# Optimization experiments

Measured on AMD Instinct MI355X. Metric: run time of the kernel, lower is better.

The kernel has to match this reference:

```python
import jax, jax.numpy as jnp
import numpy as np

N, F_IN, HID, NCLS, E = 100000, 256, 256, 32, 3200000
NHEADS, HDIM, MFEAT = 4, 64, 266  # MFEAT = int(HDIM * ln(HDIM)), performer default
ALPHA, KSTEPS, EPS = 0.1, 10, 1e-4


def setup_inputs() -> dict:
    key = jax.random.key(0)
    ks = jax.random.split(key, 16)
    p = lambda k, sh: (jax.random.normal(k, sh, dtype=jnp.float32) * 0.02)
    return {
        "x": jax.random.normal(ks[0], (N, F_IN), dtype=jnp.float32),
        "edge_index": jax.random.randint(ks[1], (2, E), 0, N, dtype=jnp.int64),
        "lin1_w": p(ks[2], (HID, F_IN)), "lin1_b": p(ks[3], (HID,)),
        "lin2_w": p(ks[4], (NCLS, 2 * HID)), "lin2_b": p(ks[5], (NCLS,)),
        "q_w": p(ks[6], (HID, F_IN)), "q_b": p(ks[7], (HID,)),
        "k_w": p(ks[8], (HID, F_IN)), "k_b": p(ks[9], (HID,)),
        "v_w": p(ks[10], (HID, F_IN)), "v_b": p(ks[11], (HID,)),
        "proj": jax.random.normal(ks[12], (MFEAT, HDIM), dtype=jnp.float32),
    }


def _softmax_kernel(data, proj, is_query):
    # performer_pytorch softmax random-feature map
    d = data.shape[-1]
    m = proj.shape[0]
    dn = d ** -0.25
    ratio = m ** -0.5
    data_dash = jnp.einsum('bhnd,md->bhnm', data * dn, proj)
    diag = 0.5 * (dn ** 2) * jnp.sum(data * data, axis=-1, keepdims=True)  # [b,h,n,1]
    if is_query:
        mx = jax.lax.stop_gradient(jnp.max(data_dash, axis=-1, keepdims=True))
    else:
        mx = jax.lax.stop_gradient(jnp.max(data_dash, axis=(-2, -1), keepdims=True))
    return ratio * (jnp.exp(data_dash - diag - mx) + EPS)


def _fast_attention(q, k, v, proj):
    # non-causal performer linear attention; q,k,v: [b,h,n,d]
    qp = _softmax_kernel(q, proj, True)   # [b,h,n,m]
    kp = _softmax_kernel(k, proj, False)  # [b,h,n,m]
    k_sum = jnp.sum(kp, axis=-2)                                   # [b,h,m]
    d_inv = 1.0 / jnp.einsum('bhnm,bhm->bhn', qp, k_sum)           # [b,h,n]
    context = jnp.einsum('bhnm,bhnd->bhmd', kp, v)                 # [b,h,m,d]
    return jnp.einsum('bhmd,bhnm,bhn->bhnd', context, qp, d_inv)   # [b,h,n,d]


def _appnp(x, edge_index, n):
    # gcn_norm with self-loops, then K iterations of x <- (1-a) A_hat x + a h
    src = jnp.concatenate([edge_index[0], jnp.arange(n, dtype=edge_index.dtype)])
    dst = jnp.concatenate([edge_index[1], jnp.arange(n, dtype=edge_index.dtype)])
    deg = jax.ops.segment_sum(jnp.ones_like(dst, dtype=x.dtype), dst, num_segments=n)
    dis = jnp.where(deg > 0, jax.lax.rsqrt(deg), 0.0)
    w = (dis[src] * dis[dst])[:, None]  # [E+N, 1]
    h = x
    for _ in range(KSTEPS):
        msg = jax.ops.segment_sum(x[src] * w, dst, num_segments=n)
        x = (1.0 - ALPHA) * msg + ALPHA * h
    return x


def reference(x, edge_index, lin1_w, lin1_b, lin2_w, lin2_b,
              q_w, q_b, k_w, k_b, v_w, v_b, proj):
    n = x.shape[0]
    # dropout layers are identity in eval mode
    xu = x[None]  # [1, N, F]
    q = (xu @ q_w.T + q_b).reshape(1, n, NHEADS, HDIM).transpose(0, 2, 1, 3)
    k = (xu @ k_w.T + k_b).reshape(1, n, NHEADS, HDIM).transpose(0, 2, 1, 3)
    v = (xu @ v_w.T + v_b).reshape(1, n, NHEADS, HDIM).transpose(0, 2, 1, 3)
    attn = _fast_attention(q, k, v, proj)                      # [1,h,n,d]
    trans = attn.transpose(0, 2, 1, 3).reshape(n, HID)         # [N, HID]
    gnn1 = x @ lin1_w.T + lin1_b                               # [N, HID]
    cat = jax.nn.elu(jnp.concatenate([gnn1, trans], axis=1))   # [N, 2*HID]
    gnn2 = jax.nn.elu(cat @ lin2_w.T + lin2_b)                 # [N, NCLS]
    final = _appnp(gnn2, edge_index, n)
    return jax.nn.log_softmax(final, axis=1), final
```

## Files before the change

kernel.cpp:

```cpp
#include <hip/hip_runtime.h>
#include <hip/hip_fp16.h>

#define NH 4
#define HD 64
#define MF 266
#define MP 288
#define NB 192
#define NBQ 128
#define DN 0.35355339059327373f
#define RATIO 0.06131393394849658f
#define EPSRF 1e-4f
#define REPS (RATIO*EPSRF)

typedef unsigned short u16;
typedef unsigned int u32;
typedef __attribute__((ext_vector_type(8))) short bf16x8;
typedef __attribute__((ext_vector_type(4))) float f32x4;
#define MFMA16(a,b,c) __builtin_amdgcn_mfma_f32_16x16x32_bf16(a,b,c,0,0,0)

__device__ __forceinline__ float bf2f(u16 u){ return __uint_as_float(((u32)u)<<16); }
__device__ __forceinline__ u16 f2bf(float f){ u32 u = __float_as_uint(f); u += 0x7FFFu + ((u>>16)&1u); return (u16)(u>>16); }
__device__ __forceinline__ u32 pack2bf(float a, float b){ return ((u32)f2bf(b)<<16) | f2bf(a); }
__device__ __forceinline__ float eluf(float x){ return x>0.f ? x : (expf(x)-1.f); }

__global__ void k_cvtw(const float* __restrict__ qw, const float* __restrict__ kw,
                       const float* __restrict__ vw, const float* __restrict__ lw,
                       const float* __restrict__ l2w, const float* __restrict__ proj,
                       u16* __restrict__ Wb, u16* __restrict__ projp, u16* __restrict__ l2wb){
  int i = blockIdx.x*256 + threadIdx.x;
  if (i < 262144){
    int sec = i>>16, r = i&65535;
    const float* s = sec==0?qw : sec==1?kw : sec==2?vw : lw;
    Wb[i] = f2bf(s[r]);
  }
  if (i < MP*64){
    int r = i>>6, c = i&63;
    projp[i] = f2bf(r < MF ? proj[r*64 + c] : 0.f);
  }
  if (i < 32*512) l2wb[i] = f2bf(l2w[i]);
}

__global__ __launch_bounds__(512,4) void k_proj(
    const float* __restrict__ x, const u16* __restrict__ Wb,
    const float* __restrict__ qb, const float* __restrict__ kb,
    const float* __restrict__ vb, const float* __restrict__ lb,
    u16* __restrict__ Q, u16* __restrict__ K, u16* __restrict__ V,
    u16* __restrict__ G1, int n)
{
  __shared__ u32 Xs[128*128];
  const int tid = threadIdx.x;
  const int w = tid>>6, l = tid&63;
  const int wr = w>>2, wc = w&3;
  const int lm = l&15, lk = l>>4;
  const int row0 = blockIdx.x*128;
  #pragma unroll 4
  for (int q=0;q<16;++q){
    int idx = q*512 + tid;
    int r = idx>>6, c4 = idx&63;
    int rr = row0 + r; if (rr > n-1) rr = n-1;
    float4 v = *(const float4*)(x + (size_t)rr*256 + c4*4);
    int word = (c4*2) ^ ((r&7)<<2);
    *(uint2*)&Xs[r*128 + word] = make_uint2(pack2bf(v.x,v.y), pack2bf(v.z,v.w));
  }
  __syncthreads();
  #pragma unroll 1
  for (int ct=0; ct<8; ++ct){
    const int c0 = ct*128 + wc*32;
    f32x4 acc[4][2] = {};
    #pragma unroll 2
    for (int kt=0; kt<8; ++kt){
      bf16x8 Af[4], Bf[2];
      #pragma unroll
      for (int jj=0;jj<2;jj++)
        Bf[jj] = *(const bf16x8*)(Wb + (size_t)(c0 + jj*16 + lm)*256 + kt*32 + lk*8);
      #pragma unroll
      for (int i=0;i<4;i++){
        const int rl = wr*64 + i*16 + lm;
        Af[i] = *(const bf16x8*)&Xs[rl*128 + ((kt*16 + lk*4) ^ ((rl&7)<<2))];
      }
      #pragma unroll
      for (int i=0;i<4;i++)
        #pragma unroll
        for (int jj=0;jj<2;jj++)
          acc[i][jj] = MFMA16(Af[i], Bf[jj], acc[i][jj]);
    }
    const int sel = c0>>8;
    const float* bp = sel==0?qb : sel==1?kb : sel==2?vb : lb;
    u16* d3 = sel==0?Q : sel==1?K : sel==2?V : G1;
    u32* dst32 = (u32*)d3;
    const bool even = (lm&1)==0;
    #pragma unroll
    for (int jj=0;jj<2;jj++){
      const int cc = (c0&255) + jj*16 + lm;
      const float bias = bp[cc];
      const int ccA = cc & ~1;
      const int hh = ccA>>6, dd = ccA&63;
      #pragma unroll
      for (int i=0;i<4;i++){
        const int rb = row0 + wr*64 + i*16 + lk*4;
        u32 m01 = pack2bf(acc[i][jj][0]+bias, acc[i][jj][1]+bias);
        u32 m23 = pack2bf(acc[i][jj][2]+bias, acc[i][jj][3]+bias);
        u32 oa = __shfl_xor(m01,1);
        u32 ob = __shfl_xor(m23,1);
        u32 wA = even ? ((m01 & 0xffffu) | ((oa & 0xffffu)<<16))
                      : ((ob  & 0xffffu) | ((m23 & 0xffffu)<<16));
        u32 wB = even ? ((m01 >> 16) | (oa & 0xffff0000u))
                      : ((ob  >> 16) | (m23 & 0xffff0000u));
        const int rA = rb + (even ? 0 : 2);
        const int rB = rA + 1;
        if (sel==3){
          if (rA < n) dst32[(size_t)rA*128 + (ccA>>1)] = wA;
          if (rB < n) dst32[(size_t)rB*128 + (ccA>>1)] = wB;
        } else {
          if (rA < n) dst32[(((size_t)hh*n + rA)<<5) + (dd>>1)] = wA;
          if (rB < n) dst32[(((size_t)hh*n + rB)<<5) + (dd>>1)] = wB;
        }
      }
    }
  }
}

__global__ void k_vcs(const u16* __restrict__ Vb, float* __restrict__ vcs, int n){
  const int h = blockIdx.y, tid = threadIdx.x;
  const int d = tid&63, seg = tid>>6;
  float s = 0.f;
  for (int node = blockIdx.x*4 + seg; node < n; node += 256)
    s += bf2f(Vb[(((size_t)h*n + node)<<6) + d]);
  __shared__ float sm[4][64];
  sm[seg][d] = s; __syncthreads();
  if (tid < 64){
    float t2 = sm[0][tid]+sm[1][tid]+sm[2][tid]+sm[3][tid];
    atomicAdd(vcs + h*64 + tid, t2);
  }
}

__global__ __launch_bounds__(256) void k_ctx(
    const u16* __restrict__ Kb, const u16* __restrict__ Vb,
    const u16* __restrict__ projp,
    float* __restrict__ ctxp, float* __restrict__ ksump,
    u32* __restrict__ kmaxg, int n)
{
  __shared__ u32 kpT[288*32];
  __shared__ u16 Vt[64][72];
  __shared__ float redk[4][288];
  const int tid = threadIdx.x;
  const int w = tid>>6, l = tid&63;
  const int bb = blockIdx.x;
  const int h = blockIdx.y;
  const int lm = l&15, lk = l>>4;
  f32x4 cacc[18] = {};
  float ksa[18] = {};
  float mreg = -3.0e38f;
  const int ntile = (n+63)>>6;
  #pragma unroll 1
  for (int t=bb; t<ntile; t+=NB){
    const int n0 = t*64;
    __syncthreads();
    #pragma unroll
    for (int q=0;q<2;q++){
      int e8 = tid + q*256;
      int nn = e8>>3, d0 = (e8&7)*8;
      uint4 rv = make_uint4(0,0,0,0);
      if (n0+nn < n) rv = *(const uint4*)(Vb + (((size_t)h*n + n0+nn)<<6) + d0);
      const u16* pv = (const u16*)&rv;
      #pragma unroll
      for (int s=0;s<8;s++) Vt[d0+s][nn] = pv[s];
    }
    int rr = n0 + w*16 + lm; if (rr > n-1) rr = n-1;
    const u16* Kbase = Kb + (((size_t)h*n + rr)<<6);
    bf16x8 af0 = *(const bf16x8*)(Kbase + lk*8);
    bf16x8 af1 = *(const bf16x8*)(Kbase + 32 + lk*8);
    float dg = 0.f;
    #pragma unroll
    for (int i2=0;i2<8;i2++){
      float a = bf2f(((const u16*)&af0)[i2]);
      float b = bf2f(((const u16*)&af1)[i2]);
      dg += a*a + b*b;
    }
    dg += __shfl_xor(dg,16); dg += __shfl_xor(dg,32);
    dg *= 0.0625f;
    float dgr[4];
    #pragma unroll
    for (int j=0;j<4;j++) dgr[j] = __shfl(dg, lk*4+j, 16);
    #pragma unroll
    for (int mt=0; mt<18; ++mt){
      bf16x8 b0 = *(const bf16x8*)(projp + (size_t)(mt*16+lm)*64 + lk*8);
      bf16x8 b1 = *(const bf16x8*)(projp + (size_t)(mt*16+lm)*64 + 32 + lk*8);
      f32x4 D = {0,0,0,0};
      D = MFMA16(af0, b0, D);
      D = MFMA16(af1, b1, D);
      const int m = mt*16 + lm;
      const bool vm = m < MF;
      float colsum = 0.f;
      u32 pk0 = 0, pk1 = 0;
      #pragma unroll
      for (int j=0;j<4;j++){
        float ddash = DN * D[j];
        float kp = 0.f;
        if (vm && (n0 + w*16 + lk*4 + j) < n){
          kp = RATIO * __expf(ddash - dgr[j]);
          mreg = fmaxf(mreg, ddash);
          colsum += kp;
        }
        if (j<2) pk0 |= ((u32)f2bf(kp)) << (16*j);
        else     pk1 |= ((u32)f2bf(kp)) << (16*(j-2));
      }
      const int wn0 = w*8 + lk*2;
      *(uint2*)&kpT[m*32 + (wn0 ^ ((m&7)<<2))] = make_uint2(pk0, pk1);
      colsum += __shfl_xor(colsum,16); colsum += __shfl_xor(colsum,32);
      ksa[mt] += colsum;
    }
    __syncthreads();
    #pragma unroll
    for (int mt=0; mt<18; ++mt){
      const int m = mt*16 + lm;
      #pragma unroll
      for (int ks=0;ks<2;++ks){
        bf16x8 a = *(const bf16x8*)&kpT[m*32 + ((ks*16 + lk*4) ^ ((m&7)<<2))];
        bf16x8 bv = *(const bf16x8*)&Vt[w*16+lm][ks*32 + lk*8];
        cacc[mt] = MFMA16(a, bv, cacc[mt]);
      }
    }
  }
  float* cp = ctxp + ((size_t)(h*NB + bb))*MP*64;
  #pragma unroll
  for (int mt=0;mt<18;++mt){
    #pragma unroll
    for (int j=0;j<4;j++){
      int m = mt*16 + lk*4 + j;
      cp[(size_t)m*64 + w*16 + lm] = cacc[mt][j];
    }
  }
  if (l < 16){
    #pragma unroll
    for (int mt=0;mt<18;++mt) redk[w][mt*16+lm] = ksa[mt];
  }
  __shared__ float redm[4];
  float mr = mreg;
  #pragma unroll
  for (int s=1;s<64;s<<=1) mr = fmaxf(mr, __shfl_xor(mr, s));
  if (l==0) redm[w] = mr;
  __syncthreads();
  for (int m2=tid; m2<MP; m2+=256){
    float s = redk[0][m2]+redk[1][m2]+redk[2][m2]+redk[3][m2];
    ksump[((size_t)(h*NB+bb))*MP + m2] = s;
  }
  if (tid==0){
    float bm = fmaxf(fmaxf(redm[0],redm[1]), fmaxf(redm[2],redm[3]));
    u32 b = __float_as_uint(bm);
    u32 enc = (b & 0x80000000u) ? ~b : (b | 0x80000000u);
    atomicMax(kmaxg + h, enc);
  }
}

__global__ void k_reduce(const float* __restrict__ ctxp, const float* __restrict__ ksump,
                         const u32* __restrict__ kmaxg, const float* __restrict__ vcs,
                         u16* __restrict__ ctxT, float* __restrict__ ksum, int n)
{
  const int T1 = NH*MP*64;
  int idx = blockIdx.x*256 + threadIdx.x;
  if (idx < T1){
    int h = idx/(MP*64), r = idx - h*MP*64, m = r>>6, d = r&63;
    u32 ee = kmaxg[h]; u32 b = (ee & 0x80000000u) ? (ee ^ 0x80000000u) : ~ee;
    float sc = __expf(-__uint_as_float(b));
    float s = 0.f;
    for (int bb=0; bb<NB; ++bb) s += ctxp[(((size_t)(h*NB+bb))*MP + m)*64 + d];
    float val = (m < MF) ? (sc*s + REPS*vcs[h*64 + d]) : 0.f;
    ctxT[((size_t)h*64 + d)*MP + m] = f2bf(val);
  } else if (idx < T1 + NH*MP){
    int k2 = idx - T1, h = k2/MP, m = k2 - h*MP;
    u32 ee = kmaxg[h]; u32 b = (ee & 0x80000000u) ? (ee ^ 0x80000000u) : ~ee;
    float sc = __expf(-__uint_as_float(b));
    float s = 0.f;
    for (int bb=0; bb<NB; ++bb) s += ksump[((size_t)(h*NB+bb))*MP + m];
    ksum[h*MP + m] = (m < MF) ? (sc*s + REPS*(float)n) : 0.f;
  }
}

__global__ __launch_bounds__(256) void k_qattn(
    const u16* __restrict__ Qb, const u16* __restrict__ projp,
    const u16* __restrict__ ctxT, const float* __restrict__ ksum,
    u16* __restrict__ trans, int n)
{
  __shared__ u32 pj[288*32];
  __shared__ u16 qp_lds[4][16][168];
  const int tid = threadIdx.x;
  const int w = tid>>6, l = tid&63;
  const int h = blockIdx.y;
  const int lm = l&15, lk = l>>4;
  #pragma unroll
  for (int q=0; q<9; ++q){
    int cix = q*256 + tid;
    int row = cix>>3, c4 = (cix&7)*4;
    uint4 v = *(const uint4*)(projp + row*64 + c4*2);
    *(uint4*)&pj[row*32 + (c4 ^ ((row&7)<<2))] = v;
  }
  float ksm[18];
  #pragma unroll
  for (int mt=0;mt<18;++mt) ksm[mt] = ksum[h*MP + mt*16 + lm];
  __syncthreads();
  const int ntile = (n+63)>>6;
  #pragma unroll 1
  for (int t = blockIdx.x; t < ntile; t += NBQ){
    const int nb = t*64 + w*16;
    int rr = nb + lm; if (rr > n-1) rr = n-1;
    const u16* Qbase = Qb + (((size_t)h*n + rr)<<6);
    bf16x8 af0 = *(const bf16x8*)(Qbase + lk*8);
    bf16x8 af1 = *(const bf16x8*)(Qbase + 32 + lk*8);
    float dg = 0.f;
    #pragma unroll
    for (int i2=0;i2<8;i2++){
      float a = bf2f(((const u16*)&af0)[i2]);
      float b = bf2f(((const u16*)&af1)[i2]);
      dg += a*a + b*b;
    }
    dg += __shfl_xor(dg,16); dg += __shfl_xor(dg,32);
    dg *= 0.0625f;
    float dgr[4];
    #pragma unroll
    for (int j=0;j<4;j++) dgr[j] = __shfl(dg, lk*4+j, 16);
    f32x4 D[18];
    #pragma unroll
    for (int mt=0;mt<18;++mt){
      const int m = mt*16 + lm;
      bf16x8 b0 = *(const bf16x8*)&pj[m*32 + ((lk*4) ^ ((m&7)<<2))];
      bf16x8 b1 = *(const bf16x8*)&pj[m*32 + ((16 + lk*4) ^ ((m&7)<<2))];
      f32x4 z = {0,0,0,0};
      z = MFMA16(af0, b0, z);
      z = MFMA16(af1, b1, z);
      D[mt] = z;
    }
    float rmax[4] = {-3.0e38f,-3.0e38f,-3.0e38f,-3.0e38f};
    #pragma unroll
    for (int mt=0;mt<17;++mt){
      const bool vm = (mt<16) || (lm<10);
      #pragma unroll
      for (int j=0;j<4;j++){
        float dd = DN*D[mt][j];
        if (vm) rmax[j] = fmaxf(rmax[j], dd);
      }
    }
    #pragma unroll
    for (int j=0;j<4;j++){
      #pragma unroll
      for (int s=1;s<16;s<<=1) rmax[j] = fmaxf(rmax[j], __shfl_xor(rmax[j], s));
    }
    float den[4] = {0,0,0,0};
    f32x4 o[4] = {{0,0,0,0},{0,0,0,0},{0,0,0,0},{0,0,0,0}};
    #pragma unroll
    for (int mt=0;mt<10;++mt){
      #pragma unroll
      for (int j=0;j<4;j++){
        float qp = RATIO*(__expf(DN*D[mt][j] - dgr[j] - rmax[j]) + EPSRF);
        den[j] += qp * ksm[mt];
        qp_lds[w][lk*4+j][mt*16+lm] = f2bf(qp);
      }
    }
    #pragma unroll
    for (int ks=0;ks<5;++ks){
      bf16x8 av = *(const bf16x8*)&qp_lds[w][lm][ks*32 + lk*8];
      #pragma unroll
      for (int dt=0;dt<4;++dt){
        bf16x8 bv = *(const bf16x8*)(ctxT + (size_t)(h*64 + dt*16 + lm)*MP + ks*32 + lk*8);
        o[dt] = MFMA16(av, bv, o[dt]);
      }
    }
    #pragma unroll
    for (int mt=10;mt<18;++mt){
      #pragma unroll
      for (int j=0;j<4;j++){
        float qp = RATIO*(__expf(DN*D[mt][j] - dgr[j] - rmax[j]) + EPSRF);
        den[j] += qp * ksm[mt];
        qp_lds[w][lk*4+j][(mt-10)*16+lm] = f2bf(qp);
      }
    }
    #pragma unroll
    for (int ks=5;ks<9;++ks){
      bf16x8 av = *(const bf16x8*)&qp_lds[w][lm][(ks-5)*32 + lk*8];
      #pragma unroll
      for (int dt=0;dt<4;++dt){
        bf16x8 bv = *(const bf16x8*)(ctxT + (size_t)(h*64 + dt*16 + lm)*MP + ks*32 + lk*8);
        o[dt] = MFMA16(av, bv, o[dt]);
      }
    }
    #pragma unroll
    for (int j=0;j<4;j++){
      #pragma unroll
      for (int s=1;s<16;s<<=1) den[j] += __shfl_xor(den[j], s);
    }
    #pragma unroll
    for (int j=0;j<4;j++){
      const int node = nb + lk*4 + j;
      if (node < n){
        const float dv = 1.f/den[j];
        #pragma unroll
        for (int dt=0;dt<4;++dt)
          trans[(size_t)node*256 + h*64 + dt*16 + lm] = f2bf(o[dt][j]*dv);
      }
    }
  }
}

__global__ __launch_bounds__(256) void k_gnn2(
    const u16* __restrict__ G1, const u16* __restrict__ trans,
    const u16* __restrict__ l2wb, const float* __restrict__ l2b,
    u16* __restrict__ xb0, int n)
{
  __shared__ u32 cat[64*256];
  const int tid = threadIdx.x;
  const int w = tid>>6, l = tid&63;
  const int lm = l&15, lk = l>>4;
  const int n0 = blockIdx.x*64;
  #pragma unroll
  for (int src=0; src<2; ++src){
    const u16* S = src ? trans : G1;
    #pragma unroll
    for (int q=0;q<8;++q){
      int idx = q*256 + tid;
      int row = idx>>5, v8 = idx&31;
      int rr = n0+row; if (rr > n-1) rr = n-1;
      uint4 raw = *(const uint4*)(S + (size_t)rr*256 + v8*8);
      const u16* p = (const u16*)&raw;
      u32 o2[4];
      #pragma unroll
      for (int t2=0;t2<4;++t2)
        o2[t2] = pack2bf(eluf(bf2f(p[t2*2])), eluf(bf2f(p[t2*2+1])));
      int word = (v8*4 + src*128) ^ ((row&7)<<2);
      *(uint4*)&cat[row*256 + word] = *(uint4*)o2;
    }
  }
  __syncthreads();
  f32x4 acc[2] = {{0,0,0,0},{0,0,0,0}};
  const int rowl = w*16 + lm;
  #pragma unroll 4
  for (int kt=0; kt<16; ++kt){
    bf16x8 a = *(const bf16x8*)&cat[rowl*256 + ((kt*16 + lk*4) ^ ((rowl&7)<<2))];
    #pragma unroll
    for (int jj=0;jj<2;++jj){
      bf16x8 b = *(const bf16x8*)(l2wb + (size_t)(jj*16+lm)*512 + kt*32 + lk*8);
      acc[jj] = MFMA16(a, b, acc[jj]);
    }
  }
  #pragma unroll
  for (int jj=0;jj<2;++jj){
    const int o = jj*16 + lm;
    const float bias = l2b[o];
    #pragma unroll
    for (int jr=0;jr<4;++jr){
      const int node = n0 + w*16 + lk*4 + jr;
      if (node < n)
        xb0[(size_t)node*32 + o] = f2bf(eluf(acc[jj][jr] + bias));
    }
  }
}

__global__ void k_edgemode(const int* __restrict__ ei, int* __restrict__ mode){
  __shared__ int any;
  if (threadIdx.x==0) any = 0;
  __syncthreads();
  if (ei[threadIdx.x*2+1] != 0) any = 1;
  __syncthreads();
  if (threadIdx.x==0) *mode = any;
}
__device__ __forceinline__ int edge_at(const int* ei, int mode, size_t idx){
  if (mode) return ei[idx];
  return (int)((const long long*)ei)[idx];
}

__global__ void k_hist(const int* __restrict__ ei, const int* __restrict__ mode,
                       u32* __restrict__ deg, int e){
  const int md = *mode;
  for (size_t i = (size_t)blockIdx.x*blockDim.x + threadIdx.x; i < (size_t)e; i += (size_t)gridDim.x*blockDim.x)
    atomicAdd(&deg[edge_at(ei, md, (size_t)e + i)], 1u);
}
__global__ void k_dis(const u32* __restrict__ deg, float* __restrict__ dis, int n){
  int i = blockIdx.x*256 + threadIdx.x;
  if (i<n) dis[i] = rsqrtf((float)(deg[i] + 1u));
}
__global__ __launch_bounds__(1024) void k_scan(const u32* __restrict__ deg, u32* __restrict__ rowp, int n){
  __shared__ u32 wsum[16];
  __shared__ u32 carry;
  const int tid = threadIdx.x, lane = tid&63, wv = tid>>6;
  if (tid==0){ carry = 0u; rowp[0] = 0u; }
  __syncthreads();
  for (int base=0; base<n; base+=1024){
    int i = base + tid;
    u32 v = (i<n)? deg[i] : 0u;
    u32 s = v;
    #pragma unroll
    for (int off=1; off<64; off<<=1){
      u32 t = __shfl_up(s, off, 64);
      if (lane >= off) s += t;
    }
    if (lane==63) wsum[wv] = s;
    __syncthreads();
    if (wv==0){
      u32 ws = (lane<16)? wsum[lane] : 0u;
      #pragma unroll
      for (int off=1; off<16; off<<=1){
        u32 t = __shfl_up(ws, off, 64);
        if (lane >= off) ws += t;
      }
      if (lane<16) wsum[lane] = ws;
    }
    __syncthreads();
    u32 pre = carry + (wv ? wsum[wv-1] : 0u);
    if (i<n) rowp[i+1] = pre + s;
    __syncthreads();
    if (tid==0) carry += wsum[15];
    __syncthreads();
  }
}
__global__ void k_copy(const u32* __restrict__ a, u32* __restrict__ b, int n){
  int i = blockIdx.x*256 + threadIdx.x; if (i<n) b[i]=a[i];
}
__global__ void k_fill(const int* __restrict__ ei, const int* __restrict__ mode,
                       const float* __restrict__ dis,
                       u32* __restrict__ cur, uint2* __restrict__ cw, int e){
  const int md = *mode;
  for (size_t i = (size_t)blockIdx.x*blockDim.x + threadIdx.x; i < (size_t)e; i += (size_t)gridDim.x*blockDim.x){
    int s = edge_at(ei, md, i);
    int t = edge_at(ei, md, (size_t)e + i);
    u32 pos = atomicAdd(&cur[t], 1u);
    cw[pos] = make_uint2((u32)s, __float_as_uint(dis[s]*dis[t]));
  }
}

__global__ __launch_bounds__(256) void k_appnp(
    const u16* __restrict__ xin, const u16* __restrict__ hb16,
    u16* __restrict__ xout, const u32* __restrict__ rowp,
    const uint2* __restrict__ cw, const float* __restrict__ dis, int n)
{
  const int g = threadIdx.x>>4, j2 = threadIdx.x&15;
  const int node = blockIdx.x*16 + g;
  if (node >= n) return;
  const u32* x32 = (const u32*)xin;
  float d0 = dis[node];
  float dd = d0*d0;
  u32 xv = x32[((size_t)node<<4) + j2];
  float a0 = dd*bf2f((u16)xv), a1 = dd*bf2f((u16)(xv>>16));
  u32 r0 = rowp[node], r1 = rowp[node+1];
  u32 k = r0;
  for (; k+4 <= r1; k += 4){
    uint2 e0 = cw[k], e1 = cw[k+1], e2 = cw[k+2], e3 = cw[k+3];
    u32 v0 = x32[((size_t)e0.x<<4)+j2], v1 = x32[((size_t)e1.x<<4)+j2];
    u32 v2 = x32[((size_t)e2.x<<4)+j2], v3 = x32[((size_t)e3.x<<4)+j2];
    float w0=__uint_as_float(e0.y), w1=__uint_as_float(e1.y);
    float w2=__uint_as_float(e2.y), w3=__uint_as_float(e3.y);
    a0 += w0*bf2f((u16)v0) + w1*bf2f((u16)v1) + w2*bf2f((u16)v2) + w3*bf2f((u16)v3);
    a1 += w0*bf2f((u16)(v0>>16)) + w1*bf2f((u16)(v1>>16)) + w2*bf2f((u16)(v2>>16)) + w3*bf2f((u16)(v3>>16));
  }
  for (; k < r1; ++k){
    uint2 e = cw[k];
    u32 v = x32[((size_t)e.x<<4)+j2];
    float wgt = __uint_as_float(e.y);
    a0 += wgt*bf2f((u16)v);
    a1 += wgt*bf2f((u16)(v>>16));
  }
  u32 hv = ((const u32*)hb16)[((size_t)node<<4) + j2];
  ((u32*)xout)[((size_t)node<<4) + j2] =
      pack2bf(0.9f*a0 + 0.1f*bf2f((u16)hv), 0.9f*a1 + 0.1f*bf2f((u16)(hv>>16)));
}

__global__ __launch_bounds__(256) void k_lsm(const u16* __restrict__ xin, float* __restrict__ out, int n){
  const int g = threadIdx.x>>5, j = threadIdx.x&31;
  const int node = blockIdx.x*8 + g;
  if (node>=n) return;
  float v = bf2f(xin[((size_t)node<<5)+j]);
  float m = v;
  #pragma unroll
  for (int o=16;o;o>>=1) m = fmaxf(m, __shfl_xor(m, o, 32));
  float s = expf(v - m);
  #pragma unroll
  for (int o=16;o;o>>=1) s += __shfl_xor(s, o, 32);
  out[((size_t)node<<5)+j] = v - m - logf(s);
  out[(size_t)n*32 + ((size_t)node<<5)+j] = v;
}

extern "C" void kernel_launch(void* const* d_in, const int* in_sizes, int n_in,
                              void* d_out, int out_size, void* d_ws, size_t ws_size,
                              hipStream_t stream)
{
  const float* x   = (const float*)d_in[0];
  const int*   ei  = (const int*)  d_in[1];
  const float* l1w = (const float*)d_in[2];
  const float* l1b = (const float*)d_in[3];
  const float* l2w = (const float*)d_in[4];
  const float* l2b = (const float*)d_in[5];
  const float* qw  = (const float*)d_in[6];
  const float* qb  = (const float*)d_in[7];
  const float* kw  = (const float*)d_in[8];
  const float* kb  = (const float*)d_in[9];
  const float* vw  = (const float*)d_in[10];
  const float* vb  = (const float*)d_in[11];
  const float* proj= (const float*)d_in[12];
  const int n = in_sizes[0] / 256;
  const int e = in_sizes[1] / 2;

  char* ws = (char*)d_ws;
  auto au = [](size_t v){ return (v + 255) & ~(size_t)255; };
  const size_t bQ = (size_t)n * 512;
  const size_t oQ = 0;
  const size_t oK = au(oQ + bQ);
  const size_t oV = au(oK + bQ);
  const size_t oG1 = au(oV + bQ);
  const size_t oCtxp = au(oG1 + bQ);
  const size_t bCtxp = (size_t)NH*NB*MP*64*4;
  const size_t oKsump = au(oCtxp + bCtxp);
  const size_t bKsump = (size_t)NH*NB*MP*4;
  const size_t oCtxT = au(oKsump + bKsump);
  const size_t oKsum = au(oCtxT + (size_t)NH*64*MP*2);
  const size_t oKmax = au(oKsum + (size_t)NH*MP*4);
  const size_t oVcs  = oKmax + 256;
  const size_t oMode = oVcs + 1024;
  const size_t oL2wb = au(oMode + 256);
  const size_t oWb   = au(oL2wb + 32768);
  const size_t oProjp= au(oWb + (size_t)1024*256*2);
  const size_t oTrans = oK;
  const size_t oG2 = oQ;
  const size_t oXb0 = au(oG2 + (size_t)n*32*4);
  const size_t oXbA = au(oXb0 + (size_t)n*32*2);
  const size_t oXbB = au(oXbA + (size_t)n*32*2);
  const size_t oDeg = au(oXbB + (size_t)n*32*2);
  const size_t oDis = au(oDeg + (size_t)n*4);
  const size_t oRowp= au(oDis + (size_t)n*4);
  const size_t oCur = au(oRowp + (size_t)(n+1)*4);
  const size_t oCw  = oV;
  (void)ws_size; (void)n_in; (void)out_size;

  u16* Q  = (u16*)(ws + oQ);
  u16* Kb = (u16*)(ws + oK);
  u16* Vb = (u16*)(ws + oV);
  u16* G1 = (u16*)(ws + oG1);
  float* ctxp = (float*)(ws + oCtxp);
  float* ksump= (float*)(ws + oKsump);
  u16*  ctxT  = (u16*)(ws + oCtxT);
  float* ksum = (float*)(ws + oKsum);
  u32*  kmax  = (u32*)(ws + oKmax);
  float* Vcs  = (float*)(ws + oVcs);
  int*  mode  = (int*)(ws + oMode);
  u16*  l2wb  = (u16*)(ws + oL2wb);
  u16*  Wb    = (u16*)(ws + oWb);
  u16*  projp = (u16*)(ws + oProjp);
  u16* trans  = (u16*)(ws + oTrans);
  u16* xb0    = (u16*)(ws + oXb0);
  u16* xbA    = (u16*)(ws + oXbA);
  u16* xbB    = (u16*)(ws + oXbB);
  u32* deg    = (u32*)(ws + oDeg);
  float* dis  = (float*)(ws + oDis);
  u32* rowp   = (u32*)(ws + oRowp);
  u32* cur    = (u32*)(ws + oCur);
  uint2* cw   = (uint2*)(ws + oCw);

  k_cvtw<<<1024,256,0,stream>>>(qw,kw,vw,l1w,l2w,proj,Wb,projp,l2wb);
  k_proj<<<(n+127)/128,512,0,stream>>>(x,Wb,qb,kb,vb,l1b,Q,Kb,Vb,G1,n);
  hipMemsetAsync(ws + oKmax, 0, 16, stream);
  hipMemsetAsync(ws + oVcs, 0, 1024, stream);
  k_vcs<<<dim3(64,4),256,0,stream>>>(Vb,Vcs,n);
  k_ctx<<<dim3(NB,NH),256,0,stream>>>(Kb,Vb,projp,ctxp,ksump,kmax,n);
  {
    int tot = NH*MP*64 + NH*MP;
    k_reduce<<<(tot+255)/256,256,0,stream>>>(ctxp,ksump,kmax,Vcs,ctxT,ksum,n);
  }
  k_qattn<<<dim3(NBQ,4),256,0,stream>>>(Q,projp,ctxT,ksum,trans,n);
  k_gnn2<<<(n+63)/64,256,0,stream>>>(G1,trans,l2wb,l2b,xb0,n);
  k_edgemode<<<1,256,0,stream>>>(ei,mode);
  hipMemsetAsync(ws + oDeg, 0, (size_t)n*4, stream);
  k_hist<<<2048,256,0,stream>>>(ei,mode,deg,e);
  k_dis<<<(n+255)/256,256,0,stream>>>(deg,dis,n);
  k_scan<<<1,1024,0,stream>>>(deg,rowp,n);
  k_copy<<<(n+255)/256,256,0,stream>>>(rowp,cur,n);
  k_fill<<<2048,256,0,stream>>>(ei,mode,dis,cur,cw,e);
  const u16* curx = xb0;
  u16* bufs[2] = {xbA, xbB};
  for (int it=0; it<10; ++it){
    u16* nxt = bufs[it&1];
    k_appnp<<<(n+15)/16,256,0,stream>>>(curx,xb0,nxt,rowp,cw,dis,n);
    curx = nxt;
  }
  k_lsm<<<(n+7)/8,256,0,stream>>>(curx,(float*)d_out,n);
}
```

Baseline: 1.522 ms.

## Shrink projection tile, widen APPNP gathers, fuse final propagation with log-softmax

```diff
diff --git a/kernel.cpp b/kernel.cpp
--- a/kernel.cpp
+++ b/kernel.cpp
@@ -40,21 +40,21 @@
   if (i < 32*512) l2wb[i] = f2bf(l2w[i]);
 }
 
-__global__ __launch_bounds__(512,4) void k_proj(
+__global__ __launch_bounds__(512,6) void k_proj(
     const float* __restrict__ x, const u16* __restrict__ Wb,
     const float* __restrict__ qb, const float* __restrict__ kb,
     const float* __restrict__ vb, const float* __restrict__ lb,
     u16* __restrict__ Q, u16* __restrict__ K, u16* __restrict__ V,
     u16* __restrict__ G1, int n)
 {
-  __shared__ u32 Xs[128*128];
+  __shared__ u32 Xs[64*128];
   const int tid = threadIdx.x;
   const int w = tid>>6, l = tid&63;
   const int wr = w>>2, wc = w&3;
   const int lm = l&15, lk = l>>4;
-  const int row0 = blockIdx.x*128;
-  #pragma unroll 4
-  for (int q=0;q<16;++q){
+  const int row0 = blockIdx.x*64;
+  #pragma unroll
+  for (int q=0;q<8;++q){
     int idx = q*512 + tid;
     int r = idx>>6, c4 = idx&63;
     int rr = row0 + r; if (rr > n-1) rr = n-1;
@@ -66,20 +66,20 @@
   #pragma unroll 1
   for (int ct=0; ct<8; ++ct){
     const int c0 = ct*128 + wc*32;
-    f32x4 acc[4][2] = {};
+    f32x4 acc[2][2] = {};
     #pragma unroll 2
     for (int kt=0; kt<8; ++kt){
-      bf16x8 Af[4], Bf[2];
+      bf16x8 Af[2], Bf[2];
       #pragma unroll
       for (int jj=0;jj<2;jj++)
         Bf[jj] = *(const bf16x8*)(Wb + (size_t)(c0 + jj*16 + lm)*256 + kt*32 + lk*8);
       #pragma unroll
-      for (int i=0;i<4;i++){
-        const int rl = wr*64 + i*16 + lm;
+      for (int i=0;i<2;i++){
+        const int rl = wr*32 + i*16 + lm;
         Af[i] = *(const bf16x8*)&Xs[rl*128 + ((kt*16 + lk*4) ^ ((rl&7)<<2))];
       }
       #pragma unroll
-      for (int i=0;i<4;i++)
+      for (int i=0;i<2;i++)
         #pragma unroll
         for (int jj=0;jj<2;jj++)
           acc[i][jj] = MFMA16(Af[i], Bf[jj], acc[i][jj]);
@@ -96,8 +96,8 @@
       const int ccA = cc & ~1;
       const int hh = ccA>>6, dd = ccA&63;
       #pragma unroll
-      for (int i=0;i<4;i++){
-        const int rb = row0 + wr*64 + i*16 + lk*4;
+      for (int i=0;i<2;i++){
+        const int rb = row0 + wr*32 + i*16 + lk*4;
         u32 m01 = pack2bf(acc[i][jj][0]+bias, acc[i][jj][1]+bias);
         u32 m23 = pack2bf(acc[i][jj][2]+bias, acc[i][jj][3]+bias);
         u32 oa = __shfl_xor(m01,1);
@@ -531,50 +531,96 @@
     u16* __restrict__ xout, const u32* __restrict__ rowp,
     const uint2* __restrict__ cw, const float* __restrict__ dis, int n)
 {
-  const int g = threadIdx.x>>4, j2 = threadIdx.x&15;
-  const int node = blockIdx.x*16 + g;
+  const int g = threadIdx.x>>3, j4 = threadIdx.x&7;
+  const int node = blockIdx.x*32 + g;
   if (node >= n) return;
-  const u32* x32 = (const u32*)xin;
+  const uint2* x64 = (const uint2*)xin;
   float d0 = dis[node];
   float dd = d0*d0;
-  u32 xv = x32[((size_t)node<<4) + j2];
-  float a0 = dd*bf2f((u16)xv), a1 = dd*bf2f((u16)(xv>>16));
+  uint2 xv = x64[((size_t)node<<3) + j4];
+  float a0 = dd*bf2f((u16)xv.x), a1 = dd*bf2f((u16)(xv.x>>16));
+  float a2 = dd*bf2f((u16)xv.y), a3 = dd*bf2f((u16)(xv.y>>16));
   u32 r0 = rowp[node], r1 = rowp[node+1];
   u32 k = r0;
   for (; k+4 <= r1; k += 4){
     uint2 e0 = cw[k], e1 = cw[k+1], e2 = cw[k+2], e3 = cw[k+3];
-    u32 v0 = x32[((size_t)e0.x<<4)+j2], v1 = x32[((size_t)e1.x<<4)+j2];
-    u32 v2 = x32[((size_t)e2.x<<4)+j2], v3 = x32[((size_t)e3.x<<4)+j2];
+    uint2 v0 = x64[((size_t)e0.x<<3)+j4], v1 = x64[((size_t)e1.x<<3)+j4];
+    uint2 v2 = x64[((size_t)e2.x<<3)+j4], v3 = x64[((size_t)e3.x<<3)+j4];
     float w0=__uint_as_float(e0.y), w1=__uint_as_float(e1.y);
     float w2=__uint_as_float(e2.y), w3=__uint_as_float(e3.y);
-    a0 += w0*bf2f((u16)v0) + w1*bf2f((u16)v1) + w2*bf2f((u16)v2) + w3*bf2f((u16)v3);
-    a1 += w0*bf2f((u16)(v0>>16)) + w1*bf2f((u16)(v1>>16)) + w2*bf2f((u16)(v2>>16)) + w3*bf2f((u16)(v3>>16));
+    a0 += w0*bf2f((u16)v0.x) + w1*bf2f((u16)v1.x) + w2*bf2f((u16)v2.x) + w3*bf2f((u16)v3.x);
+    a1 += w0*bf2f((u16)(v0.x>>16)) + w1*bf2f((u16)(v1.x>>16)) + w2*bf2f((u16)(v2.x>>16)) + w3*bf2f((u16)(v3.x>>16));
+    a2 += w0*bf2f((u16)v0.y) + w1*bf2f((u16)v1.y) + w2*bf2f((u16)v2.y) + w3*bf2f((u16)v3.y);
+    a3 += w0*bf2f((u16)(v0.y>>16)) + w1*bf2f((u16)(v1.y>>16)) + w2*bf2f((u16)(v2.y>>16)) + w3*bf2f((u16)(v3.y>>16));
   }
   for (; k < r1; ++k){
     uint2 e = cw[k];
-    u32 v = x32[((size_t)e.x<<4)+j2];
+    uint2 v = x64[((size_t)e.x<<3)+j4];
     float wgt = __uint_as_float(e.y);
-    a0 += wgt*bf2f((u16)v);
-    a1 += wgt*bf2f((u16)(v>>16));
-  }
-  u32 hv = ((const u32*)hb16)[((size_t)node<<4) + j2];
-  ((u32*)xout)[((size_t)node<<4) + j2] =
-      pack2bf(0.9f*a0 + 0.1f*bf2f((u16)hv), 0.9f*a1 + 0.1f*bf2f((u16)(hv>>16)));
-}
-
-__global__ __launch_bounds__(256) void k_lsm(const u16* __restrict__ xin, float* __restrict__ out, int n){
-  const int g = threadIdx.x>>5, j = threadIdx.x&31;
-  const int node = blockIdx.x*8 + g;
-  if (node>=n) return;
-  float v = bf2f(xin[((size_t)node<<5)+j]);
-  float m = v;
-  #pragma unroll
-  for (int o=16;o;o>>=1) m = fmaxf(m, __shfl_xor(m, o, 32));
-  float s = expf(v - m);
-  #pragma unroll
-  for (int o=16;o;o>>=1) s += __shfl_xor(s, o, 32);
-  out[((size_t)node<<5)+j] = v - m - logf(s);
-  out[(size_t)n*32 + ((size_t)node<<5)+j] = v;
+    a0 += wgt*bf2f((u16)v.x);
+    a1 += wgt*bf2f((u16)(v.x>>16));
+    a2 += wgt*bf2f((u16)v.y);
+    a3 += wgt*bf2f((u16)(v.y>>16));
+  }
+  uint2 hv = ((const uint2*)hb16)[((size_t)node<<3) + j4];
+  uint2 o;
+  o.x = pack2bf(0.9f*a0 + 0.1f*bf2f((u16)hv.x), 0.9f*a1 + 0.1f*bf2f((u16)(hv.x>>16)));
+  o.y = pack2bf(0.9f*a2 + 0.1f*bf2f((u16)hv.y), 0.9f*a3 + 0.1f*bf2f((u16)(hv.y>>16)));
+  ((uint2*)xout)[((size_t)node<<3) + j4] = o;
+}
+
+__global__ __launch_bounds__(256) void k_appnp_lsm(
+    const u16* __restrict__ xin, const u16* __restrict__ hb16,
+    float* __restrict__ out, const u32* __restrict__ rowp,
+    const uint2* __restrict__ cw, const float* __restrict__ dis, int n)
+{
+  const int g = threadIdx.x>>3, j4 = threadIdx.x&7;
+  const int node = blockIdx.x*32 + g;
+  if (node >= n) return;
+  const uint2* x64 = (const uint2*)xin;
+  float d0 = dis[node];
+  float dd = d0*d0;
+  uint2 xv = x64[((size_t)node<<3) + j4];
+  float a0 = dd*bf2f((u16)xv.x), a1 = dd*bf2f((u16)(xv.x>>16));
+  float a2 = dd*bf2f((u16)xv.y), a3 = dd*bf2f((u16)(xv.y>>16));
+  u32 r0 = rowp[node], r1 = rowp[node+1];
+  u32 k = r0;
+  for (; k+4 <= r1; k += 4){
+    uint2 e0 = cw[k], e1 = cw[k+1], e2 = cw[k+2], e3 = cw[k+3];
+    uint2 v0 = x64[((size_t)e0.x<<3)+j4], v1 = x64[((size_t)e1.x<<3)+j4];
+    uint2 v2 = x64[((size_t)e2.x<<3)+j4], v3 = x64[((size_t)e3.x<<3)+j4];
+    float w0=__uint_as_float(e0.y), w1=__uint_as_float(e1.y);
+    float w2=__uint_as_float(e2.y), w3=__uint_as_float(e3.y);
+    a0 += w0*bf2f((u16)v0.x) + w1*bf2f((u16)v1.x) + w2*bf2f((u16)v2.x) + w3*bf2f((u16)v3.x);
+    a1 += w0*bf2f((u16)(v0.x>>16)) + w1*bf2f((u16)(v1.x>>16)) + w2*bf2f((u16)(v2.x>>16)) + w3*bf2f((u16)(v3.x>>16));
+    a2 += w0*bf2f((u16)v0.y) + w1*bf2f((u16)v1.y) + w2*bf2f((u16)v2.y) + w3*bf2f((u16)v3.y);
+    a3 += w0*bf2f((u16)(v0.y>>16)) + w1*bf2f((u16)(v1.y>>16)) + w2*bf2f((u16)(v2.y>>16)) + w3*bf2f((u16)(v3.y>>16));
+  }
+  for (; k < r1; ++k){
+    uint2 e = cw[k];
+    uint2 v = x64[((size_t)e.x<<3)+j4];
+    float wgt = __uint_as_float(e.y);
+    a0 += wgt*bf2f((u16)v.x);
+    a1 += wgt*bf2f((u16)(v.x>>16));
+    a2 += wgt*bf2f((u16)v.y);
+    a3 += wgt*bf2f((u16)(v.y>>16));
+  }
+  uint2 hv = ((const uint2*)hb16)[((size_t)node<<3) + j4];
+  float v0 = 0.9f*a0 + 0.1f*bf2f((u16)hv.x);
+  float v1 = 0.9f*a1 + 0.1f*bf2f((u16)(hv.x>>16));
+  float v2 = 0.9f*a2 + 0.1f*bf2f((u16)hv.y);
+  float v3 = 0.9f*a3 + 0.1f*bf2f((u16)(hv.y>>16));
+  float m = fmaxf(fmaxf(v0,v1), fmaxf(v2,v3));
+  #pragma unroll
+  for (int o2=1;o2<8;o2<<=1) m = fmaxf(m, __shfl_xor(m, o2, 8));
+  float s = __expf(v0-m)+__expf(v1-m)+__expf(v2-m)+__expf(v3-m);
+  #pragma unroll
+  for (int o2=1;o2<8;o2<<=1) s += __shfl_xor(s, o2, 8);
+  float ls = m + logf(s);
+  float4 lsv = make_float4(v0-ls, v1-ls, v2-ls, v3-ls);
+  *(float4*)(out + (size_t)node*32 + j4*4) = lsv;
+  float4 raw = make_float4(v0, v1, v2, v3);
+  *(float4*)(out + (size_t)n*32 + (size_t)node*32 + j4*4) = raw;
 }
 
 extern "C" void kernel_launch(void* const* d_in, const int* in_sizes, int n_in,
@@ -653,7 +699,7 @@
   uint2* cw   = (uint2*)(ws + oCw);
 
   k_cvtw<<<1024,256,0,stream>>>(qw,kw,vw,l1w,l2w,proj,Wb,projp,l2wb);
-  k_proj<<<(n+127)/128,512,0,stream>>>(x,Wb,qb,kb,vb,l1b,Q,Kb,Vb,G1,n);
+  k_proj<<<(n+63)/64,512,0,stream>>>(x,Wb,qb,kb,vb,l1b,Q,Kb,Vb,G1,n);
   hipMemsetAsync(ws + oKmax, 0, 16, stream);
   hipMemsetAsync(ws + oVcs, 0, 1024, stream);
   k_vcs<<<dim3(64,4),256,0,stream>>>(Vb,Vcs,n);
@@ -673,10 +719,10 @@
   k_fill<<<2048,256,0,stream>>>(ei,mode,dis,cur,cw,e);
   const u16* curx = xb0;
   u16* bufs[2] = {xbA, xbB};
-  for (int it=0; it<10; ++it){
+  for (int it=0; it<9; ++it){
     u16* nxt = bufs[it&1];
-    k_appnp<<<(n+15)/16,256,0,stream>>>(curx,xb0,nxt,rowp,cw,dis,n);
+    k_appnp<<<(n+31)/32,256,0,stream>>>(curx,xb0,nxt,rowp,cw,dis,n);
     curx = nxt;
   }
-  k_lsm<<<(n+7)/8,256,0,stream>>>(curx,(float*)d_out,n);
-}
+  k_appnp_lsm<<<(n+31)/32,256,0,stream>>>(curx,xb0,(float*)d_out,rowp,cw,dis,n);
+}
```

Result: slower. 1.576 ms (+3.5%).
